# Kernel tuning notes

Hardware: AMD Instinct MI355X
Metric: run time of the kernel (lower is better)

Reference implementation:

```python
import jax, jax.numpy as jnp
import numpy as np
import math

B, S, D, H = 2, 2048, 1024, 16
DK = D // H


def setup_inputs() -> dict:
    key = jax.random.key(0)
    k1, k2, k3, k4, k5, k6 = jax.random.split(key, 6)
    scale = 1.0 / math.sqrt(D)
    return {
        "query": jax.random.normal(k1, (B, S, D), dtype=jnp.float32),
        "key": jax.random.normal(k2, (B, S, D), dtype=jnp.float32),
        "value": jax.random.normal(k3, (B, S, D), dtype=jnp.float32),
        "Wqkv": jax.random.normal(k4, (D, D), dtype=jnp.float32) * scale,
        "Wout": jax.random.normal(k5, (D, D), dtype=jnp.float32) * scale,
        "mask": jax.random.randint(k6, (B, 1, S, S), 0, 2, dtype=jnp.int32),
    }


def reference(query, key, value, Wqkv, Wout, mask):
    # Single shared QKV projection (same weight applied to q, k, v), no bias.
    q = query @ Wqkv.T
    k = key @ Wqkv.T
    v = value @ Wqkv.T
    # Faithful to the original: reshape (B, S, D) -> (B, H, S, DK) directly
    # (torch .reshape(n_batches, h, -1, d_k), NOT view+transpose).
    q = q.reshape(B, H, S, DK)
    k = k.reshape(B, H, S, DK)
    v = v.reshape(B, H, S, DK)
    scores = jnp.einsum("bhqd,bhkd->bhqk", q, k) / math.sqrt(DK)
    scores = jnp.where(mask == 0, jnp.float32(-1e9), scores)
    p_attn = jax.nn.softmax(scores, axis=-1)  # dropout is identity in eval
    x = jnp.einsum("bhqk,bhkd->bhqd", p_attn, v)  # [B,H,S,DK]
    x = x.transpose(0, 2, 1, 3).reshape(B, S, H * DK)
    return x @ Wout.T
```

## Files before the change

kernel.cpp:

```cpp
#include <hip/hip_runtime.h>
#include <stdint.h>


typedef __bf16 bf16;
typedef __bf16 bf16x8 __attribute__((ext_vector_type(8)));
typedef __bf16 bf16x4 __attribute__((ext_vector_type(4)));
typedef float f32x4 __attribute__((ext_vector_type(4)));

#define MFMA16(a, b, c) __builtin_amdgcn_mfma_f32_16x16x32_bf16((a), (b), (c), 0, 0, 0)
#define EXP2(x) __builtin_amdgcn_exp2f(x)

static constexpr int BATCH = 2;
static constexpr int SEQ = 2048;
static constexpr int DIM = 1024;
static constexpr int DK = 64;
static constexpr float QSCALE = 0.125f * 1.44269504088896340736f;

__device__ inline void gload16(const void* g, void* l) {
  __builtin_amdgcn_global_load_lds((const __attribute__((address_space(1))) void*)g,
                                   (__attribute__((address_space(3))) void*)l, 16, 0, 0);
}

__global__ __launch_bounds__(256) void mask_bits_kernel(const int* __restrict__ mask,
                                                        unsigned long long* __restrict__ bits) {
  int idx = blockIdx.x * 256 + threadIdx.x;
  int m = mask[idx];
  unsigned long long bal = __ballot(m != 0);
  if ((threadIdx.x & 63) == 0) bits[idx >> 6] = bal;
}

__global__ __launch_bounds__(256) void cvt_bf16_kernel(const float* __restrict__ s0,
                                                       const float* __restrict__ s1,
                                                       const float* __restrict__ s2,
                                                       const float* __restrict__ s3,
                                                       const float* __restrict__ s4,
                                                       bf16* __restrict__ d0, bf16* __restrict__ d1,
                                                       bf16* __restrict__ d2, bf16* __restrict__ d3,
                                                       bf16* __restrict__ d4) {
  const int y = blockIdx.y;
  const float* s = (y == 0) ? s0 : (y == 1) ? s1 : (y == 2) ? s2 : (y == 3) ? s3 : s4;
  bf16* d = (y == 0) ? d0 : (y == 1) ? d1 : (y == 2) ? d2 : (y == 3) ? d3 : d4;
  const int n8 = (y < 3) ? (BATCH * SEQ * DIM / 8) : (DIM * DIM / 8);
  for (int i = blockIdx.x * 256 + threadIdx.x; i < n8; i += gridDim.x * 256) {
    const float4 a = ((const float4*)s)[2 * i];
    const float4 b = ((const float4*)s)[2 * i + 1];
    bf16x8 v;
    v[0] = (bf16)a.x;
    v[1] = (bf16)a.y;
    v[2] = (bf16)a.z;
    v[3] = (bf16)a.w;
    v[4] = (bf16)b.x;
    v[5] = (bf16)b.y;
    v[6] = (bf16)b.z;
    v[7] = (bf16)b.w;
    ((bf16x8*)d)[i] = v;
  }
}

template <int BM, int NBY, int NBZ, typename TC>
__global__ __launch_bounds__(256, (BM == 128) ? 3 : 2) void gemm_bt_lds(
    const bf16* __restrict__ A0, const bf16* __restrict__ A1, const bf16* __restrict__ A2,
    const bf16* __restrict__ W, TC* __restrict__ C0, TC* __restrict__ C1, TC* __restrict__ C2,
    float scale0) {
  constexpr int K = 1024, N = 1024;
  constexpr int MT = BM / 32;
  constexpr int NB = 8 * NBY * NBZ;
  __shared__ __align__(16) bf16 As[2][BM * 32];
  __shared__ __align__(16) bf16 Bs[2][128 * 32];

  const int lin = blockIdx.x + 8 * (blockIdx.y + NBY * blockIdx.z);
  const int l = (lin & 7) * (NB / 8) + (lin >> 3);
  const int lx = l & 7;
  const int lyz = l >> 3;
  const int ly = lyz % NBY;
  const int lz = lyz / NBY;

  const bf16* A = (lz == 0) ? A0 : (lz == 1) ? A1 : A2;
  TC* C = (lz == 0) ? C0 : (lz == 1) ? C1 : C2;
  const float sc = (lz == 0) ? scale0 : 1.0f;

  const int tid = threadIdx.x;
  const int lane = tid & 63;
  const int wv = tid >> 6;
  const int wm = wv >> 1, wn = wv & 1;
  const int lrow = lane & 15, quad = lane >> 4;
  const int m0 = ly * BM, n0 = lx * 128;

  const int r0 = tid >> 2;
  const int c0 = (((tid & 3) ^ ((r0 >> 1) & 3)) * 8);
  const bf16* pa0 = A + (size_t)(m0 + r0) * K + c0;
  const bf16* pb0 = W + (size_t)(n0 + r0) * K + c0;
  const bf16* pb1 = W + (size_t)(n0 + 64 + r0) * K + c0;
  const bf16* pa1 = nullptr;
  if constexpr (BM == 128) pa1 = A + (size_t)(m0 + 64 + r0) * K + c0;

  const f32x4 fz = {0.f, 0.f, 0.f, 0.f};
  f32x4 acc[MT][4];
#pragma unroll
  for (int i = 0; i < MT; ++i)
#pragma unroll
    for (int j = 0; j < 4; ++j) acc[i][j] = fz;

  const int sw = (lrow >> 1) & 3;
  const int rb = (quad ^ sw) * 8;

  gload16(pa0, &As[0][tid * 8]);
  if constexpr (BM == 128) gload16(pa1, &As[0][2048 + tid * 8]);
  gload16(pb0, &Bs[0][tid * 8]);
  gload16(pb1, &Bs[0][2048 + tid * 8]);
  __syncthreads();

  for (int t = 0; t < K / 32; ++t) {
    const int cur = t & 1;
    if (t + 1 < K / 32) {
      const int k1 = (t + 1) * 32;
      gload16(pa0 + k1, &As[cur ^ 1][tid * 8]);
      if constexpr (BM == 128) gload16(pa1 + k1, &As[cur ^ 1][2048 + tid * 8]);
      gload16(pb0 + k1, &Bs[cur ^ 1][tid * 8]);
      gload16(pb1 + k1, &Bs[cur ^ 1][2048 + tid * 8]);
    }
    bf16x8 af[MT], bfr[4];
#pragma unroll
    for (int mt = 0; mt < MT; ++mt)
      af[mt] = *(const bf16x8*)(&As[cur][(wm * (BM / 2) + mt * 16 + lrow) * 32 + rb]);
#pragma unroll
    for (int nt = 0; nt < 4; ++nt)
      bfr[nt] = *(const bf16x8*)(&Bs[cur][(wn * 64 + nt * 16 + lrow) * 32 + rb]);
#pragma unroll
    for (int mt = 0; mt < MT; ++mt)
#pragma unroll
      for (int nt = 0; nt < 4; ++nt) acc[mt][nt] = MFMA16(af[mt], bfr[nt], acc[mt][nt]);
    __syncthreads();
  }

#pragma unroll
  for (int mt = 0; mt < MT; ++mt) {
    const int gm = m0 + wm * (BM / 2) + mt * 16 + quad * 4;
#pragma unroll
    for (int nt = 0; nt < 4; ++nt) {
      const int gn = n0 + wn * 64 + nt * 16 + lrow;
#pragma unroll
      for (int r = 0; r < 4; ++r) C[(size_t)(gm + r) * N + gn] = (TC)(acc[mt][nt][r] * sc);
    }
  }
}

__global__ __launch_bounds__(256, 2) void attn_kernel(const bf16* __restrict__ Qg,
                                                      const bf16* __restrict__ Kg,
                                                      const bf16* __restrict__ Vg,
                                                      const unsigned* __restrict__ bits,
                                                      bf16* __restrict__ Y) {
  constexpr int LQ = 72;
  __shared__ bf16 Qs[128 * LQ];
  __shared__ bf16 Ks[64 * LQ];
  __shared__ bf16 Vts[64 * LQ];
  __shared__ bf16 Ps[4][32 * LQ];

  const int tid = threadIdx.x;
  const int lane = tid & 63;
  const int wv = tid >> 6;
  const int lrow = lane & 15, quad = lane >> 4;
  const int bh = blockIdx.y;
  const int b = bh >> 4, h = bh & 15;
  const int q0 = blockIdx.x * 128;

  const bf16* Qh = Qg + (size_t)bh * (SEQ * DK);
  const bf16* Kh = Kg + (size_t)bh * (SEQ * DK);
  const bf16* Vh = Vg + (size_t)bh * (SEQ * DK);

#pragma unroll
  for (int i = 0; i < 4; ++i) {
    int s = tid + i * 256;
    int row = s >> 3, c8 = (s & 7) * 8;
    *(uint4*)(&Qs[row * LQ + c8]) = *(const uint4*)(Qh + (size_t)(q0 + row) * DK + c8);
  }

  const int krow = tid >> 3;
  const int kc8 = (tid & 7) * 8;
  const bf16* pk0 = Kh + (size_t)krow * DK + kc8;
  const bf16* pk1 = Kh + (size_t)(krow + 32) * DK + kc8;
  const int vn2 = tid & 31;
  const int vk2b = tid >> 5;
  const bf16* pv0 = Vh + (size_t)(vk2b + 0) * 2 * DK + vn2 * 2;
  const bf16* pv1 = Vh + (size_t)(vk2b + 8) * 2 * DK + vn2 * 2;
  const bf16* pv2 = Vh + (size_t)(vk2b + 16) * 2 * DK + vn2 * 2;
  const bf16* pv3 = Vh + (size_t)(vk2b + 24) * 2 * DK + vn2 * 2;

  uint4 kr0, kr1;
  uint32_t va[4], vb[4];

  kr0 = *(const uint4*)(pk0);
  kr1 = *(const uint4*)(pk1);
  va[0] = *(const uint32_t*)(pv0);
  vb[0] = *(const uint32_t*)(pv0 + DK);
  va[1] = *(const uint32_t*)(pv1);
  vb[1] = *(const uint32_t*)(pv1 + DK);
  va[2] = *(const uint32_t*)(pv2);
  vb[2] = *(const uint32_t*)(pv2 + DK);
  va[3] = *(const uint32_t*)(pv3);
  vb[3] = *(const uint32_t*)(pv3 + DK);
  *(uint4*)(&Ks[krow * LQ + kc8]) = kr0;
  *(uint4*)(&Ks[(krow + 32) * LQ + kc8]) = kr1;
#pragma unroll
  for (int i = 0; i < 4; ++i) {
    uint32_t t0 = (va[i] & 0xffffu) | (vb[i] << 16);
    uint32_t t1 = (va[i] >> 16) | (vb[i] & 0xffff0000u);
    *(uint32_t*)(&Vts[(vn2 * 2) * LQ + (vk2b + i * 8) * 2]) = t0;
    *(uint32_t*)(&Vts[(vn2 * 2 + 1) * LQ + (vk2b + i * 8) * 2]) = t1;
  }
  __syncthreads();

  bf16x8 qf[2][2];
#pragma unroll
  for (int nt = 0; nt < 2; ++nt)
#pragma unroll
    for (int ks = 0; ks < 2; ++ks)
      qf[nt][ks] = *(const bf16x8*)(&Qs[(wv * 32 + nt * 16 + lrow) * LQ + ks * 32 + quad * 8]);
  __syncthreads();

  const f32x4 fz = {0.f, 0.f, 0.f, 0.f};
  f32x4 of_t[4][2];
#pragma unroll
  for (int i = 0; i < 4; ++i)
#pragma unroll
    for (int j = 0; j < 2; ++j) of_t[i][j] = fz;
  float lsum[2] = {0.f, 0.f};

  const unsigned* bitrow = bits + (size_t)b * SEQ * (SEQ / 32);

  for (int kt = 0; kt < 32; ++kt) {
    const int cur = kt & 1;
    bf16* kb = cur ? Qs : Ks;
    bf16* vbuf = cur ? (Qs + 64 * LQ) : Vts;
    if (kt + 1 < 32) {
      const size_t adv = (size_t)(kt + 1) * 64 * DK;
      kr0 = *(const uint4*)(pk0 + adv);
      kr1 = *(const uint4*)(pk1 + adv);
      va[0] = *(const uint32_t*)(pv0 + adv);
      vb[0] = *(const uint32_t*)(pv0 + adv + DK);
      va[1] = *(const uint32_t*)(pv1 + adv);
      vb[1] = *(const uint32_t*)(pv1 + adv + DK);
      va[2] = *(const uint32_t*)(pv2 + adv);
      vb[2] = *(const uint32_t*)(pv2 + adv + DK);
      va[3] = *(const uint32_t*)(pv3 + adv);
      vb[3] = *(const uint32_t*)(pv3 + adv + DK);
    }
    uint2 mwn[2];
#pragma unroll
    for (int nt = 0; nt < 2; ++nt) {
      int row = q0 + wv * 32 + nt * 16 + lrow;
      mwn[nt] = *(const uint2*)(bitrow + (size_t)row * (SEQ / 32) + kt * 2);
    }

    f32x4 st[4][2];
#pragma unroll
    for (int mt = 0; mt < 4; ++mt)
#pragma unroll
      for (int nt = 0; nt < 2; ++nt) st[mt][nt] = fz;
#pragma unroll
    for (int ks = 0; ks < 2; ++ks) {
#pragma unroll
      for (int mt = 0; mt < 4; ++mt) {
        bf16x8 kfv = *(const bf16x8*)(kb + (mt * 16 + lrow) * LQ + ks * 32 + quad * 8);
#pragma unroll
        for (int nt = 0; nt < 2; ++nt) st[mt][nt] = MFMA16(kfv, qf[nt][ks], st[mt][nt]);
      }
    }

#pragma unroll
    for (int nt = 0; nt < 2; ++nt) {
      uint32_t ux = mwn[nt].x >> (quad * 4);
      uint32_t uy = mwn[nt].y >> (quad * 4);
      float psum = 0.f;
#pragma unroll
      for (int mt = 0; mt < 4; ++mt) {
        uint32_t u = (mt & 2) ? uy : ux;
        int sh = (mt & 1) << 4;
        bf16x4 pk;
#pragma unroll
        for (int r = 0; r < 4; ++r) {
          float p = EXP2(st[mt][nt][r]);
          p = ((u >> (sh + r)) & 1u) ? p : 0.f;
          psum += p;
          pk[r] = (bf16)p;
        }
        *(bf16x4*)(&Ps[wv][(nt * 16 + lrow) * LQ + mt * 16 + quad * 4]) = pk;
      }
      lsum[nt] += psum;
    }

#pragma unroll
    for (int ks = 0; ks < 2; ++ks) {
      bf16x8 avf[4], bpf[2];
#pragma unroll
      for (int dkt = 0; dkt < 4; ++dkt)
        avf[dkt] = *(const bf16x8*)(vbuf + (dkt * 16 + lrow) * LQ + ks * 32 + quad * 8);
#pragma unroll
      for (int rt = 0; rt < 2; ++rt)
        bpf[rt] = *(const bf16x8*)(&Ps[wv][(rt * 16 + lrow) * LQ + ks * 32 + quad * 8]);
#pragma unroll
      for (int dkt = 0; dkt < 4; ++dkt)
#pragma unroll
        for (int rt = 0; rt < 2; ++rt) of_t[dkt][rt] = MFMA16(avf[dkt], bpf[rt], of_t[dkt][rt]);
    }

    if (kt + 1 < 32) {
      bf16* kbn = cur ? Ks : Qs;
      bf16* vbn = cur ? Vts : (Qs + 64 * LQ);
      *(uint4*)(kbn + krow * LQ + kc8) = kr0;
      *(uint4*)(kbn + (krow + 32) * LQ + kc8) = kr1;
#pragma unroll
      for (int i = 0; i < 4; ++i) {
        uint32_t t0 = (va[i] & 0xffffu) | (vb[i] << 16);
        uint32_t t1 = (va[i] >> 16) | (vb[i] & 0xffff0000u);
        *(uint32_t*)(vbn + (vn2 * 2) * LQ + (vk2b + i * 8) * 2) = t0;
        *(uint32_t*)(vbn + (vn2 * 2 + 1) * LQ + (vk2b + i * 8) * 2) = t1;
      }
    }
    __syncthreads();
  }

  float linv[2];
#pragma unroll
  for (int nt = 0; nt < 2; ++nt) {
    float v = lsum[nt];
    v += __shfl_xor(v, 16);
    v += __shfl_xor(v, 32);
    linv[nt] = 1.0f / fmaxf(v, 1e-20f);
  }

#pragma unroll
  for (int dkt = 0; dkt < 4; ++dkt)
#pragma unroll
    for (int rt = 0; rt < 2; ++rt) {
      bf16x4 o;
#pragma unroll
      for (int j = 0; j < 4; ++j) o[j] = (bf16)(of_t[dkt][rt][j] * linv[rt]);
      const int row = q0 + wv * 32 + rt * 16 + lrow;
      *(bf16x4*)(&Y[((size_t)b * SEQ + row) * DIM + h * 64 + dkt * 16 + quad * 4]) = o;
    }
}

extern "C" void kernel_launch(void* const* d_in, const int* in_sizes, int n_in,
                              void* d_out, int out_size, void* d_ws, size_t ws_size,
                              hipStream_t stream) {
  const float* query = (const float*)d_in[0];
  const float* key = (const float*)d_in[1];
  const float* value = (const float*)d_in[2];
  const float* Wqkv = (const float*)d_in[3];
  const float* Wout = (const float*)d_in[4];
  const int* mask = (const int*)d_in[5];
  float* out = (float*)d_out;

  char* ws = (char*)d_ws;
  bf16* qin = (bf16*)(ws);
  bf16* kin = (bf16*)(ws + 8388608);
  bf16* vin = (bf16*)(ws + 16777216);
  bf16* Wq = (bf16*)(ws + 25165824);
  bf16* Wo = (bf16*)(ws + 27262976);
  bf16* q = (bf16*)(ws + 29360128);
  bf16* k = (bf16*)(ws + 37748736);
  bf16* v = (bf16*)(ws + 46137344);
  bf16* y = (bf16*)(ws);
  unsigned long long* bits64 = (unsigned long long*)(ws + 54525952);

  mask_bits_kernel<<<(BATCH * SEQ * SEQ) / 256, 256, 0, stream>>>(mask, bits64);

  cvt_bf16_kernel<<<dim3(256, 5), 256, 0, stream>>>(query, key, value, Wqkv, Wout,
                                                    qin, kin, vin, Wq, Wo);

  gemm_bt_lds<128, 32, 3, bf16>
      <<<dim3(8, 32, 3), 256, 0, stream>>>(qin, kin, vin, Wq, q, k, v, QSCALE);

  attn_kernel<<<dim3(16, 32), 256, 0, stream>>>(q, k, v, (const unsigned*)bits64, y);

  gemm_bt_lds<64, 64, 1, float>
      <<<dim3(8, 64, 1), 256, 0, stream>>>(y, y, y, Wo, out, out, out, 1.0f);
}
```

Measured before the change: 253.1 us.

## Fuse mask/convert prep kernels and enlarge QKV GEMM tile to 128x256

Merges the mask-bitpacking and fp32-to-bf16 conversion kernels into one flat-grid prep kernel, removing a launch and the grid-stride loop. Generalizes the GEMM over BN and uses a 128x256 tile for the QKV projection, doubling per-block reuse and MFMA work per LDS load at the cost of more accumulator registers and lower occupancy. Also drops the LDS XOR swizzle on the A/B tiles, which may bring back bank conflicts.

```diff
diff --git a/kernel.cpp b/kernel.cpp
--- a/kernel.cpp
+++ b/kernel.cpp
@@ -21,59 +21,74 @@
                                    (__attribute__((address_space(3))) void*)l, 16, 0, 0);
 }
 
-__global__ __launch_bounds__(256) void mask_bits_kernel(const int* __restrict__ mask,
-                                                        unsigned long long* __restrict__ bits) {
-  int idx = blockIdx.x * 256 + threadIdx.x;
-  int m = mask[idx];
-  unsigned long long bal = __ballot(m != 0);
-  if ((threadIdx.x & 63) == 0) bits[idx >> 6] = bal;
-}
-
-__global__ __launch_bounds__(256) void cvt_bf16_kernel(const float* __restrict__ s0,
-                                                       const float* __restrict__ s1,
-                                                       const float* __restrict__ s2,
-                                                       const float* __restrict__ s3,
-                                                       const float* __restrict__ s4,
-                                                       bf16* __restrict__ d0, bf16* __restrict__ d1,
-                                                       bf16* __restrict__ d2, bf16* __restrict__ d3,
-                                                       bf16* __restrict__ d4) {
-  const int y = blockIdx.y;
-  const float* s = (y == 0) ? s0 : (y == 1) ? s1 : (y == 2) ? s2 : (y == 3) ? s3 : s4;
-  bf16* d = (y == 0) ? d0 : (y == 1) ? d1 : (y == 2) ? d2 : (y == 3) ? d3 : d4;
-  const int n8 = (y < 3) ? (BATCH * SEQ * DIM / 8) : (DIM * DIM / 8);
-  for (int i = blockIdx.x * 256 + threadIdx.x; i < n8; i += gridDim.x * 256) {
-    const float4 a = ((const float4*)s)[2 * i];
-    const float4 b = ((const float4*)s)[2 * i + 1];
-    bf16x8 v;
-    v[0] = (bf16)a.x;
-    v[1] = (bf16)a.y;
-    v[2] = (bf16)a.z;
-    v[3] = (bf16)a.w;
-    v[4] = (bf16)b.x;
-    v[5] = (bf16)b.y;
-    v[6] = (bf16)b.z;
-    v[7] = (bf16)b.w;
-    ((bf16x8*)d)[i] = v;
-  }
-}
-
-template <int BM, int NBY, int NBZ, typename TC>
-__global__ __launch_bounds__(256, (BM == 128) ? 3 : 2) void gemm_bt_lds(
+__global__ __launch_bounds__(256) void prep_kernel(
+    const int* __restrict__ mask, unsigned long long* __restrict__ bits,
+    const float* __restrict__ sq, const float* __restrict__ sk, const float* __restrict__ sv,
+    const float* __restrict__ swq, const float* __restrict__ swo,
+    bf16* __restrict__ dq, bf16* __restrict__ dk, bf16* __restrict__ dv,
+    bf16* __restrict__ dwq, bf16* __restrict__ dwo) {
+  const int bid = blockIdx.x;
+  const int tid = threadIdx.x;
+  if (bid < 8192) {
+    const int lane = tid & 63, wv = tid >> 6;
+    const int ebase = (bid * 4 + wv) * 256;
+    unsigned long long w[4];
+#pragma unroll
+    for (int j = 0; j < 4; ++j) {
+      int m = mask[ebase + j * 64 + lane];
+      w[j] = __ballot(m != 0);
+    }
+    if (lane == 0) {
+#pragma unroll
+      for (int j = 0; j < 4; ++j) bits[(ebase >> 6) + j] = w[j];
+    }
+    return;
+  }
+  int r = bid - 8192;
+  const float* s;
+  bf16* d;
+  int i;
+  if (r < 6144) {
+    s = (r < 2048) ? sq : (r < 4096) ? sk : sv;
+    d = (r < 2048) ? dq : (r < 4096) ? dk : dv;
+    i = (r & 2047) * 256 + tid;
+  } else {
+    r -= 6144;
+    s = (r < 512) ? swq : swo;
+    d = (r < 512) ? dwq : dwo;
+    i = (r & 511) * 256 + tid;
+  }
+  const float4 a = ((const float4*)s)[2 * i];
+  const float4 b = ((const float4*)s)[2 * i + 1];
+  bf16x8 v;
+  v[0] = (bf16)a.x;
+  v[1] = (bf16)a.y;
+  v[2] = (bf16)a.z;
+  v[3] = (bf16)a.w;
+  v[4] = (bf16)b.x;
+  v[5] = (bf16)b.y;
+  v[6] = (bf16)b.z;
+  v[7] = (bf16)b.w;
+  ((bf16x8*)d)[i] = v;
+}
+
+template <int BM, int BN, int NBX, int NBY, int NBZ, typename TC>
+__global__ __launch_bounds__(256, 2) void gemm_bt_lds(
     const bf16* __restrict__ A0, const bf16* __restrict__ A1, const bf16* __restrict__ A2,
     const bf16* __restrict__ W, TC* __restrict__ C0, TC* __restrict__ C1, TC* __restrict__ C2,
     float scale0) {
   constexpr int K = 1024, N = 1024;
-  constexpr int MT = BM / 32;
-  constexpr int NB = 8 * NBY * NBZ;
+  constexpr int MT = BM / 32, NT = BN / 32;
+  constexpr int SA = BM / 64, SB = BN / 64;
+  constexpr int NB = NBX * NBY * NBZ;
   __shared__ __align__(16) bf16 As[2][BM * 32];
-  __shared__ __align__(16) bf16 Bs[2][128 * 32];
-
-  const int lin = blockIdx.x + 8 * (blockIdx.y + NBY * blockIdx.z);
+  __shared__ __align__(16) bf16 Bs[2][BN * 32];
+
+  const int lin = blockIdx.x + NBX * (blockIdx.y + NBY * blockIdx.z);
   const int l = (lin & 7) * (NB / 8) + (lin >> 3);
-  const int lx = l & 7;
-  const int lyz = l >> 3;
-  const int ly = lyz % NBY;
-  const int lz = lyz / NBY;
+  const int lx = l % NBX;
+  const int ly = (l / NBX) % NBY;
+  const int lz = l / (NBX * NBY);
 
   const bf16* A = (lz == 0) ? A0 : (lz == 1) ? A1 : A2;
   TC* C = (lz == 0) ? C0 : (lz == 1) ? C1 : C2;
@@ -84,52 +99,49 @@
   const int wv = tid >> 6;
   const int wm = wv >> 1, wn = wv & 1;
   const int lrow = lane & 15, quad = lane >> 4;
-  const int m0 = ly * BM, n0 = lx * 128;
-
-  const int r0 = tid >> 2;
-  const int c0 = (((tid & 3) ^ ((r0 >> 1) & 3)) * 8);
-  const bf16* pa0 = A + (size_t)(m0 + r0) * K + c0;
-  const bf16* pb0 = W + (size_t)(n0 + r0) * K + c0;
-  const bf16* pb1 = W + (size_t)(n0 + 64 + r0) * K + c0;
-  const bf16* pa1 = nullptr;
-  if constexpr (BM == 128) pa1 = A + (size_t)(m0 + 64 + r0) * K + c0;
+  const int m0 = ly * BM, n0 = lx * BN;
+
+  const int r0 = tid >> 2, c0 = (tid & 3) * 8;
+  const bf16* pa[SA];
+  const bf16* pb[SB];
+#pragma unroll
+  for (int s = 0; s < SA; ++s) pa[s] = A + (size_t)(m0 + s * 64 + r0) * K + c0;
+#pragma unroll
+  for (int s = 0; s < SB; ++s) pb[s] = W + (size_t)(n0 + s * 64 + r0) * K + c0;
 
   const f32x4 fz = {0.f, 0.f, 0.f, 0.f};
-  f32x4 acc[MT][4];
+  f32x4 acc[MT][NT];
 #pragma unroll
   for (int i = 0; i < MT; ++i)
 #pragma unroll
-    for (int j = 0; j < 4; ++j) acc[i][j] = fz;
-
-  const int sw = (lrow >> 1) & 3;
-  const int rb = (quad ^ sw) * 8;
-
-  gload16(pa0, &As[0][tid * 8]);
-  if constexpr (BM == 128) gload16(pa1, &As[0][2048 + tid * 8]);
-  gload16(pb0, &Bs[0][tid * 8]);
-  gload16(pb1, &Bs[0][2048 + tid * 8]);
+    for (int j = 0; j < NT; ++j) acc[i][j] = fz;
+
+#pragma unroll
+  for (int s = 0; s < SA; ++s) gload16(pa[s], &As[0][s * 2048 + tid * 8]);
+#pragma unroll
+  for (int s = 0; s < SB; ++s) gload16(pb[s], &Bs[0][s * 2048 + tid * 8]);
   __syncthreads();
 
   for (int t = 0; t < K / 32; ++t) {
     const int cur = t & 1;
     if (t + 1 < K / 32) {
       const int k1 = (t + 1) * 32;
-      gload16(pa0 + k1, &As[cur ^ 1][tid * 8]);
-      if constexpr (BM == 128) gload16(pa1 + k1, &As[cur ^ 1][2048 + tid * 8]);
-      gload16(pb0 + k1, &Bs[cur ^ 1][tid * 8]);
-      gload16(pb1 + k1, &Bs[cur ^ 1][2048 + tid * 8]);
-    }
-    bf16x8 af[MT], bfr[4];
+#pragma unroll
+      for (int s = 0; s < SA; ++s) gload16(pa[s] + k1, &As[cur ^ 1][s * 2048 + tid * 8]);
+#pragma unroll
+      for (int s = 0; s < SB; ++s) gload16(pb[s] + k1, &Bs[cur ^ 1][s * 2048 + tid * 8]);
+    }
+    bf16x8 af[MT], bfr[NT];
 #pragma unroll
     for (int mt = 0; mt < MT; ++mt)
-      af[mt] = *(const bf16x8*)(&As[cur][(wm * (BM / 2) + mt * 16 + lrow) * 32 + rb]);
-#pragma unroll
-    for (int nt = 0; nt < 4; ++nt)
-      bfr[nt] = *(const bf16x8*)(&Bs[cur][(wn * 64 + nt * 16 + lrow) * 32 + rb]);
+      af[mt] = *(const bf16x8*)(&As[cur][(wm * (BM / 2) + mt * 16 + lrow) * 32 + quad * 8]);
+#pragma unroll
+    for (int nt = 0; nt < NT; ++nt)
+      bfr[nt] = *(const bf16x8*)(&Bs[cur][(wn * (BN / 2) + nt * 16 + lrow) * 32 + quad * 8]);
 #pragma unroll
     for (int mt = 0; mt < MT; ++mt)
 #pragma unroll
-      for (int nt = 0; nt < 4; ++nt) acc[mt][nt] = MFMA16(af[mt], bfr[nt], acc[mt][nt]);
+      for (int nt = 0; nt < NT; ++nt) acc[mt][nt] = MFMA16(af[mt], bfr[nt], acc[mt][nt]);
     __syncthreads();
   }
 
@@ -137,8 +149,8 @@
   for (int mt = 0; mt < MT; ++mt) {
     const int gm = m0 + wm * (BM / 2) + mt * 16 + quad * 4;
 #pragma unroll
-    for (int nt = 0; nt < 4; ++nt) {
-      const int gn = n0 + wn * 64 + nt * 16 + lrow;
+    for (int nt = 0; nt < NT; ++nt) {
+      const int gn = n0 + wn * (BN / 2) + nt * 16 + lrow;
 #pragma unroll
       for (int r = 0; r < 4; ++r) C[(size_t)(gm + r) * N + gn] = (TC)(acc[mt][nt][r] * sc);
     }
@@ -364,16 +376,14 @@
   bf16* y = (bf16*)(ws);
   unsigned long long* bits64 = (unsigned long long*)(ws + 54525952);
 
-  mask_bits_kernel<<<(BATCH * SEQ * SEQ) / 256, 256, 0, stream>>>(mask, bits64);
-
-  cvt_bf16_kernel<<<dim3(256, 5), 256, 0, stream>>>(query, key, value, Wqkv, Wout,
-                                                    qin, kin, vin, Wq, Wo);
-
-  gemm_bt_lds<128, 32, 3, bf16>
-      <<<dim3(8, 32, 3), 256, 0, stream>>>(qin, kin, vin, Wq, q, k, v, QSCALE);
+  prep_kernel<<<15360, 256, 0, stream>>>(mask, bits64, query, key, value, Wqkv, Wout,
+                                         qin, kin, vin, Wq, Wo);
+
+  gemm_bt_lds<128, 256, 4, 32, 3, bf16>
+      <<<dim3(4, 32, 3), 256, 0, stream>>>(qin, kin, vin, Wq, q, k, v, QSCALE);
 
   attn_kernel<<<dim3(16, 32), 256, 0, stream>>>(q, k, v, (const unsigned*)bits64, y);
 
-  gemm_bt_lds<64, 64, 1, float>
+  gemm_bt_lds<64, 128, 8, 64, 1, float>
       <<<dim3(8, 64, 1), 256, 0, stream>>>(y, y, y, Wo, out, out, out, 1.0f);
 }
```

Measured after the change: 255.8 us. No clear change (+1.1%).
